# Kernel optimization log

Measured on AMD Instinct MI355X. Metric: run time of the kernel, lower is better.

Reference implementation:

```python
import jax, jax.numpy as jnp
import numpy as np

N_PARTICLES = 100000
STATE_DIM = 64          # 3 + 2*2 + 57
MSG_OUT = 64
HIDDEN = 32
N_EDGES = 1600000


def _init_linear(key, fan_in, fan_out):
    kw, kb = jax.random.split(key)
    bound = 1.0 / np.sqrt(fan_in)
    W = jax.random.uniform(kw, (fan_in, fan_out), minval=-bound, maxval=bound, dtype=jnp.float32)
    b = jax.random.uniform(kb, (fan_out,), minval=-bound, maxval=bound, dtype=jnp.float32)
    return W, b


def setup_inputs() -> dict:
    key = jax.random.key(0)
    ks = jax.random.split(key, 8)
    x = jax.random.normal(ks[0], (N_PARTICLES, STATE_DIM), dtype=jnp.float32)
    edge_index = jax.random.randint(ks[1], (2, N_EDGES), 0, N_PARTICLES, dtype=jnp.int64)
    # message conv MLP: [2*STATE_DIM] -> 32 -> 32 -> MSG_OUT
    mW1, mb1 = _init_linear(ks[2], 2 * STATE_DIM, HIDDEN)
    mW2, mb2 = _init_linear(ks[3], HIDDEN, HIDDEN)
    mW3, mb3 = _init_linear(ks[4], HIDDEN, MSG_OUT)
    # own_state_nn MLP: [STATE_DIM + MSG_OUT] -> 32 -> 32 -> STATE_DIM
    oW1, ob1 = _init_linear(ks[5], STATE_DIM + MSG_OUT, HIDDEN)
    oW2, ob2 = _init_linear(ks[6], HIDDEN, HIDDEN)
    oW3, ob3 = _init_linear(ks[7], HIDDEN, STATE_DIM)
    return {"x": x, "edge_index": edge_index,
            "mW1": mW1, "mb1": mb1, "mW2": mW2, "mb2": mb2, "mW3": mW3, "mb3": mb3,
            "oW1": oW1, "ob1": ob1, "oW2": oW2, "ob2": ob2, "oW3": oW3, "ob3": ob3}


def _mlp3(h, W1, b1, W2, b2, W3, b3):
    h = jax.nn.relu(h @ W1 + b1)
    h = jax.nn.relu(h @ W2 + b2)
    return h @ W3 + b3


def reference(x, edge_index, mW1, mb1, mW2, mb2, mW3, mb3,
              oW1, ob1, oW2, ob2, oW3, ob3):
    src, dst = edge_index[0], edge_index[1]
    # edge-wise message: MLP over [x_src || x_dst]  -> [E, MSG_OUT]
    e_feat = jnp.concatenate([x[src], x[dst]], axis=-1)  # [E, 2*STATE_DIM]
    m = _mlp3(e_feat, mW1, mb1, mW2, mb2, mW3, mb3)
    # scatter-sum aggregation at destination node
    messages = jax.ops.segment_sum(m, dst, num_segments=x.shape[0])  # [N, MSG_OUT]
    combined = jnp.concatenate([x, messages], axis=-1)  # [N, STATE_DIM+MSG_OUT]
    new_state = _mlp3(combined, oW1, ob1, oW2, ob2, oW3, ob3)
    return new_state
```

## Files before the change

kernel.cpp:

```cpp
#include <hip/hip_runtime.h>

#define NP 100000
#define NE 1600000
#define SD 64
#define HID 32
#define MSG 64
#define NP_PAD 100352
#define NTILE (NP / 16)
#define TILE_BLOCKS ((NTILE + 3) / 4)
#define BINSZ 512
#define NBIN ((NP + BINSZ - 1) / BINSZ)
#define EPW 8192
#define NWG ((NE + EPW - 1) / EPW)

typedef float v4f __attribute__((ext_vector_type(4)));
typedef short v4s __attribute__((ext_vector_type(4)));
typedef short v8s __attribute__((ext_vector_type(8)));
typedef __bf16 v8bf __attribute__((ext_vector_type(8)));

#define WQ_FRAGS 56

__device__ __forceinline__ v4f MFMA32(v8s a, v8s b, v4f c) {
  return __builtin_amdgcn_mfma_f32_16x16x32_bf16(
      __builtin_bit_cast(v8bf, a), __builtin_bit_cast(v8bf, b), c, 0, 0, 0);
}

__device__ __forceinline__ short f2bf(float f) {
  return __builtin_bit_cast(short, (__bf16)f);
}
__device__ __forceinline__ float bf2f(short s) {
  unsigned u = ((unsigned)(unsigned short)s) << 16;
  return __builtin_bit_cast(float, u);
}

__device__ __forceinline__ v4f mfma3(v8s ah, v8s al, v8s bh, v8s bl, v4f c) {
  c = MFMA32(al, bh, c);
  c = MFMA32(ah, bl, c);
  c = MFMA32(ah, bh, c);
  return c;
}

__device__ __forceinline__ void load_wfrag(const float* __restrict__ W, int ld,
                                           int kb, int m0, int lq, int l15,
                                           v8s* hi, v8s* lo) {
  v8s h, l;
#pragma unroll
  for (int j = 0; j < 8; ++j) {
    int k = kb + ((j < 4) ? (4 * lq + j) : (16 + 4 * lq + (j - 4)));
    float v = W[k * ld + m0 + l15];
    short hb = f2bf(v);
    h[j] = hb;
    l[j] = f2bf(v - bf2f(hb));
  }
  *hi = h;
  *lo = l;
}

__device__ __forceinline__ void split8(v4f a, v4f b, v8s* hi, v8s* lo) {
  v8s h, l;
#pragma unroll
  for (int j = 0; j < 4; ++j) {
    short ha = f2bf(a[j]); h[j] = ha; l[j] = f2bf(a[j] - bf2f(ha));
    short hb = f2bf(b[j]); h[j + 4] = hb; l[j + 4] = f2bf(b[j] - bf2f(hb));
  }
  *hi = h;
  *lo = l;
}

__device__ __forceinline__ void load_xfrag(const float* xs, int kb, int lq,
                                           v8s* hi, v8s* lo) {
  v4f a = *reinterpret_cast<const v4f*>(xs + kb + 4 * lq);
  v4f b = *reinterpret_cast<const v4f*>(xs + kb + 16 + 4 * lq);
  split8(a, b, hi, lo);
}

__device__ __forceinline__ void chain_frag(v4f d0, v4f d1, v8s* hi, v8s* lo) {
  v4f a, b;
#pragma unroll
  for (int j = 0; j < 4; ++j) {
    a[j] = fmaxf(d0[j], 0.f);
    b[j] = fmaxf(d1[j], 0.f);
  }
  split8(a, b, hi, lo);
}

__global__ __launch_bounds__(256, 2) void setup_kernel(
    const float* __restrict__ x, const int* __restrict__ ei,
    const float* __restrict__ mW1, const float* __restrict__ mb1,
    const float* __restrict__ mW2, const float* __restrict__ mW3,
    const float* __restrict__ oW1, const float* __restrict__ oW2,
    const float* __restrict__ oW3,
    int* __restrict__ gOff, short* __restrict__ wqs,
    float* __restrict__ h1d_buf, short* __restrict__ h1s_buf) {
  __shared__ int cnt[NBIN];
  const int blk = blockIdx.x;

  if (blk < NWG) {
    for (int i = threadIdx.x; i < NBIN; i += 256) cnt[i] = 0;
    __syncthreads();
    const int e0 = blk * EPW;
    const int e1 = (e0 + EPW < NE) ? e0 + EPW : NE;
    for (int e = e0 + threadIdx.x; e < e1; e += 256)
      atomicAdd(&cnt[ei[NE + e] >> 9], 1);
    __syncthreads();
    for (int i = threadIdx.x; i < NBIN; i += 256) gOff[i * NWG + blk] = cnt[i];
    return;
  }

  const int lane = threadIdx.x & 63;
  const int l15 = lane & 15;
  const int lq = lane >> 4;

  if (blk == NWG) {
    if (threadIdx.x >= 64) return;
    v8s* wq = reinterpret_cast<v8s*>(wqs);
    v8s h, l;
#pragma unroll
    for (int t = 0; t < 2; ++t)
#pragma unroll
      for (int kc = 0; kc < 2; ++kc) {
        load_wfrag(mW1, HID, kc * 32, t * 16, lq, l15, &h, &l);
        wq[(t * 2 + kc) * 64 + lane] = h;
        wq[(4 + t * 2 + kc) * 64 + lane] = l;
        load_wfrag(mW1, HID, 64 + kc * 32, t * 16, lq, l15, &h, &l);
        wq[(8 + t * 2 + kc) * 64 + lane] = h;
        wq[(12 + t * 2 + kc) * 64 + lane] = l;
      }
#pragma unroll
    for (int t = 0; t < 2; ++t) {
      load_wfrag(mW2, HID, 0, t * 16, lq, l15, &h, &l);
      wq[(16 + t) * 64 + lane] = h;
      wq[(18 + t) * 64 + lane] = l;
    }
#pragma unroll
    for (int t = 0; t < 4; ++t) {
      load_wfrag(mW3, MSG, 0, t * 16, lq, l15, &h, &l);
      wq[(20 + t) * 64 + lane] = h;
      wq[(24 + t) * 64 + lane] = l;
    }
#pragma unroll
    for (int t = 0; t < 2; ++t)
#pragma unroll
      for (int kc = 0; kc < 4; ++kc) {
        load_wfrag(oW1, HID, kc * 32, t * 16, lq, l15, &h, &l);
        wq[(28 + t * 4 + kc) * 64 + lane] = h;
        wq[(36 + t * 4 + kc) * 64 + lane] = l;
      }
#pragma unroll
    for (int t = 0; t < 2; ++t) {
      load_wfrag(oW2, HID, 0, t * 16, lq, l15, &h, &l);
      wq[(44 + t) * 64 + lane] = h;
      wq[(46 + t) * 64 + lane] = l;
    }
#pragma unroll
    for (int t = 0; t < 4; ++t) {
      load_wfrag(oW3, SD, 0, t * 16, lq, l15, &h, &l);
      wq[(48 + t) * 64 + lane] = h;
      wq[(52 + t) * 64 + lane] = l;
    }
    return;
  }

  const int tile = ((blk - NWG - 1) * 256 + (int)threadIdx.x) >> 6;
  if (tile >= NTILE) return;
  const int node = tile * 16 + l15;

  v4f d0, d1, s0 = {0.f, 0.f, 0.f, 0.f}, s1 = {0.f, 0.f, 0.f, 0.f};
#pragma unroll
  for (int q = 0; q < 4; ++q) {
    d0[q] = mb1[4 * lq + q];
    d1[q] = mb1[16 + 4 * lq + q];
  }
#pragma unroll
  for (int kc = 0; kc < 2; ++kc) {
    v8s xh, xl, wh, wl;
    load_xfrag(x + (size_t)node * SD, kc * 32, lq, &xh, &xl);
    load_wfrag(mW1, HID, 64 + kc * 32, 0, lq, l15, &wh, &wl);
    d0 = mfma3(wh, wl, xh, xl, d0);
    load_wfrag(mW1, HID, 64 + kc * 32, 16, lq, l15, &wh, &wl);
    d1 = mfma3(wh, wl, xh, xl, d1);
    load_wfrag(mW1, HID, kc * 32, 0, lq, l15, &wh, &wl);
    s0 = mfma3(wh, wl, xh, xl, s0);
    load_wfrag(mW1, HID, kc * 32, 16, lq, l15, &wh, &wl);
    s1 = mfma3(wh, wl, xh, xl, s1);
  }
  *reinterpret_cast<v4f*>(h1d_buf + (size_t)node * HID + 4 * lq) = d0;
  *reinterpret_cast<v4f*>(h1d_buf + (size_t)node * HID + 16 + 4 * lq) = d1;
  v4s q0, q1;
#pragma unroll
  for (int q = 0; q < 4; ++q) {
    q0[q] = f2bf(s0[q]);
    q1[q] = f2bf(s1[q]);
  }
  *reinterpret_cast<v4s*>(h1s_buf + (size_t)node * HID + 4 * lq) = q0;
  *reinterpret_cast<v4s*>(h1s_buf + (size_t)node * HID + 16 + 4 * lq) = q1;
}


__global__ __launch_bounds__(256) void scan_bins_kernel(
    int* __restrict__ gOff, int* __restrict__ binStart) {
  __shared__ int tot[NBIN];
  const int b = threadIdx.x;
  if (b < NBIN) {
    int run = 0;
    for (int w = 0; w < NWG; ++w) {
      int v = gOff[b * NWG + w];
      gOff[b * NWG + w] = run;
      run += v;
    }
    tot[b] = run;
  }
  __syncthreads();
  if (threadIdx.x == 0) {
    int run = 0;
    for (int bb = 0; bb < NBIN; ++bb) {
      binStart[bb] = run;
      run += tot[bb];
    }
    binStart[NBIN] = run;
  }
  __syncthreads();
  if (b < NBIN) {
    int base = binStart[b];
    for (int w = 0; w < NWG; ++w) gOff[b * NWG + w] += base;
  }
}

__global__ __launch_bounds__(256) void bin_scatter_kernel(
    const int* __restrict__ ei, const int* __restrict__ gOff,
    int2* __restrict__ pairs) {
  __shared__ int cur[NBIN];
  const int w = blockIdx.x;
  for (int i = threadIdx.x; i < NBIN; i += 256) cur[i] = gOff[i * NWG + w];
  __syncthreads();
  const int e0 = w * EPW;
  const int e1 = (e0 + EPW < NE) ? e0 + EPW : NE;
  for (int e = e0 + threadIdx.x; e < e1; e += 256) {
    int s = ei[e];
    int d = ei[NE + e];
    int pos = atomicAdd(&cur[d >> 9], 1);
    pairs[pos] = make_int2(s, d);
  }
}

__global__ __launch_bounds__(512) void bin_csr_kernel(
    const int2* __restrict__ pairs, const int* __restrict__ binStart,
    int2* __restrict__ co, int* __restrict__ csr_src) {
  __shared__ int sh[BINSZ];
  __shared__ int cu[BINSZ];
  const int b = blockIdx.x;
  const int t = threadIdx.x;
  cu[t] = 0;
  __syncthreads();
  const int p0 = binStart[b], p1 = binStart[b + 1];
  for (int p = p0 + t; p < p1; p += BINSZ)
    atomicAdd(&cu[pairs[p].y & (BINSZ - 1)], 1);
  __syncthreads();
  const int v = cu[t];
  sh[t] = v;
  __syncthreads();
  for (int off = 1; off < BINSZ; off <<= 1) {
    int a = (t >= off) ? sh[t - off] : 0;
    __syncthreads();
    sh[t] += a;
    __syncthreads();
  }
  const int excl = sh[t] - v;
  const int node = b * BINSZ + t;
  if (node < NP) co[node] = make_int2(p0 + excl, v);
  cu[t] = excl;
  __syncthreads();
  for (int p = p0 + t; p < p1; p += BINSZ) {
    int2 pr = pairs[p];
    int loc = atomicAdd(&cu[pr.y & (BINSZ - 1)], 1);
    csr_src[p0 + loc] = pr.x;
  }
}

__global__ __launch_bounds__(256, 4) void edge_mfma_kernel(
    const short* __restrict__ h1s, const float* __restrict__ h1d_buf,
    const short* __restrict__ wqs, const int2* __restrict__ co,
    const int* __restrict__ csr_src, const float* __restrict__ mb2,
    float* __restrict__ rsum) {
  const int lane = threadIdx.x & 63;
  const int l15 = lane & 15;
  const int lq = lane >> 4;
  const int wid = (blockIdx.x * 256 + threadIdx.x) >> 6;
  const int nw = gridDim.x * 4;
  const v8s* wq = reinterpret_cast<const v8s*>(wqs);

  const v8s w2h0 = wq[16 * 64 + lane], w2h1 = wq[17 * 64 + lane];
  const v8s w2l0 = wq[18 * 64 + lane], w2l1 = wq[19 * 64 + lane];
  v4f bb0, bb1;
#pragma unroll
  for (int q = 0; q < 4; ++q) {
    bb0[q] = mb2[4 * lq + q];
    bb1[q] = mb2[16 + 4 * lq + q];
  }

  for (int n = wid; n < NP; n += nw) {
    const int2 c = co[n];
    const int off = c.x, cnt = c.y;
    const int ng = (cnt + 15) >> 4;

    const v4f h1d0 = *reinterpret_cast<const v4f*>(h1d_buf + (size_t)n * HID + 4 * lq);
    const v4f h1d1 = *reinterpret_cast<const v4f*>(h1d_buf + (size_t)n * HID + 16 + 4 * lq);

    v4f r0 = {0.f, 0.f, 0.f, 0.f}, r1 = {0.f, 0.f, 0.f, 0.f};

    int sa = (l15 < cnt) ? csr_src[off + l15] : 0;
    v4s a0 = *reinterpret_cast<const v4s*>(h1s + (size_t)sa * HID + 4 * lq);
    v4s b0 = *reinterpret_cast<const v4s*>(h1s + (size_t)sa * HID + 16 + 4 * lq);
    int sb = (l15 < cnt - 16) ? csr_src[off + 16 + l15] : 0;
    v4s a1 = *reinterpret_cast<const v4s*>(h1s + (size_t)sb * HID + 4 * lq);
    v4s b1 = *reinterpret_cast<const v4s*>(h1s + (size_t)sb * HID + 16 + 4 * lq);

    int rem = cnt;
    for (int g = 0; g < ng; ++g) {
      int sc = (l15 < rem - 32) ? csr_src[off + (g + 2) * 16 + l15] : 0;

      v4f d0, d1;
#pragma unroll
      for (int q = 0; q < 4; ++q) {
        d0[q] = h1d0[q] + bf2f(a0[q]);
        d1[q] = h1d1[q] + bf2f(b0[q]);
      }

      v8s ph, pl;
      chain_frag(d0, d1, &ph, &pl);
      v4f e0 = bb0, e1 = bb1;
      e0 = mfma3(w2h0, w2l0, ph, pl, e0);
      e1 = mfma3(w2h1, w2l1, ph, pl, e1);

      if (l15 < rem) {
#pragma unroll
        for (int j = 0; j < 4; ++j) {
          r0[j] += fmaxf(e0[j], 0.f);
          r1[j] += fmaxf(e1[j], 0.f);
        }
      }

      v4s a2 = *reinterpret_cast<const v4s*>(h1s + (size_t)sc * HID + 4 * lq);
      v4s b2 = *reinterpret_cast<const v4s*>(h1s + (size_t)sc * HID + 16 + 4 * lq);

      a0 = a1; b0 = b1;
      a1 = a2; b1 = b2;
      rem -= 16;
    }

#pragma unroll
    for (int j = 0; j < 4; ++j) {
      float a = r0[j], b = r1[j];
      a += __shfl_xor(a, 1); a += __shfl_xor(a, 2);
      a += __shfl_xor(a, 4); a += __shfl_xor(a, 8);
      b += __shfl_xor(b, 1); b += __shfl_xor(b, 2);
      b += __shfl_xor(b, 4); b += __shfl_xor(b, 8);
      r0[j] = a; r1[j] = b;
    }
    if (l15 == 0) {
      *reinterpret_cast<v4f*>(rsum + (size_t)n * HID + 4 * lq) = r0;
      *reinterpret_cast<v4f*>(rsum + (size_t)n * HID + 16 + 4 * lq) = r1;
    }
  }
}

__global__ __launch_bounds__(256, 2) void fused_tail_kernel(
    const float* __restrict__ x, const short* __restrict__ wqs,
    const float* __restrict__ rsum, const int2* __restrict__ co,
    const float* __restrict__ mb3,
    const float* __restrict__ ob1, const float* __restrict__ ob2,
    const float* __restrict__ ob3,
    float* __restrict__ out) {
  const int lane = threadIdx.x & 63;
  const int l15 = lane & 15;
  const int lq = lane >> 4;
  const int tile = (blockIdx.x * 256 + threadIdx.x) >> 6;
  if (tile >= NTILE) return;
  const v8s* wq = reinterpret_cast<const v8s*>(wqs);

  const int node = tile * 16 + l15;
  const float fc = (float)co[node].y;

  v4f ra = *reinterpret_cast<const v4f*>(rsum + (size_t)node * HID + 4 * lq);
  v4f rb = *reinterpret_cast<const v4f*>(rsum + (size_t)node * HID + 16 + 4 * lq);
  v8s bh, bl;
  split8(ra, rb, &bh, &bl);

  v4f m[4];
#pragma unroll
  for (int t = 0; t < 4; ++t) {
    v4f c = {0.f, 0.f, 0.f, 0.f};
    c = mfma3(wq[(20 + t) * 64 + lane], wq[(24 + t) * 64 + lane], bh, bl, c);
#pragma unroll
    for (int q = 0; q < 4; ++q) c[q] += fc * mb3[t * 16 + 4 * lq + q];
    m[t] = c;
  }

  v4f d0, d1;
#pragma unroll
  for (int q = 0; q < 4; ++q) {
    d0[q] = ob1[4 * lq + q];
    d1[q] = ob1[16 + 4 * lq + q];
  }
#pragma unroll
  for (int kc = 0; kc < 2; ++kc) {
    v8s xh, xl;
    load_xfrag(x + (size_t)node * SD, kc * 32, lq, &xh, &xl);
    d0 = mfma3(wq[(28 + kc) * 64 + lane], wq[(36 + kc) * 64 + lane], xh, xl, d0);
    d1 = mfma3(wq[(32 + kc) * 64 + lane], wq[(40 + kc) * 64 + lane], xh, xl, d1);
  }
#pragma unroll
  for (int kc = 0; kc < 2; ++kc) {
    v8s mh, ml;
    split8(m[kc * 2], m[kc * 2 + 1], &mh, &ml);
    d0 = mfma3(wq[(30 + kc) * 64 + lane], wq[(38 + kc) * 64 + lane], mh, ml, d0);
    d1 = mfma3(wq[(34 + kc) * 64 + lane], wq[(42 + kc) * 64 + lane], mh, ml, d1);
  }

  v8s ph, pl;
  chain_frag(d0, d1, &ph, &pl);
  v4f e0, e1;
#pragma unroll
  for (int q = 0; q < 4; ++q) {
    e0[q] = ob2[4 * lq + q];
    e1[q] = ob2[16 + 4 * lq + q];
  }
  e0 = mfma3(wq[44 * 64 + lane], wq[46 * 64 + lane], ph, pl, e0);
  e1 = mfma3(wq[45 * 64 + lane], wq[47 * 64 + lane], ph, pl, e1);

  v8s rh, rl;
  chain_frag(e0, e1, &rh, &rl);
  float* orow = out + (size_t)node * SD;
#pragma unroll
  for (int t = 0; t < 4; ++t) {
    v4f c;
#pragma unroll
    for (int q = 0; q < 4; ++q) c[q] = ob3[t * 16 + 4 * lq + q];
    c = mfma3(wq[(48 + t) * 64 + lane], wq[(52 + t) * 64 + lane], rh, rl, c);
    *reinterpret_cast<v4f*>(orow + t * 16 + 4 * lq) = c;
  }
}

extern "C" void kernel_launch(void* const* d_in, const int* in_sizes, int n_in,
                              void* d_out, int out_size, void* d_ws,
                              size_t ws_size, hipStream_t stream) {
  const float* x = (const float*)d_in[0];
  const int* ei = (const int*)d_in[1];
  const float* mW1 = (const float*)d_in[2];
  const float* mb1 = (const float*)d_in[3];
  const float* mW2 = (const float*)d_in[4];
  const float* mb2 = (const float*)d_in[5];
  const float* mW3 = (const float*)d_in[6];
  const float* mb3 = (const float*)d_in[7];
  const float* oW1 = (const float*)d_in[8];
  const float* ob1 = (const float*)d_in[9];
  const float* oW2 = (const float*)d_in[10];
  const float* ob2 = (const float*)d_in[11];
  const float* oW3 = (const float*)d_in[12];
  const float* ob3 = (const float*)d_in[13];
  float* out = (float*)d_out;

  float* h1d_buf = (float*)d_out;
  short* h1s_buf = (short*)((char*)d_out + (size_t)NP * HID * 4);

  char* p = (char*)d_ws;
  short* wqs = (short*)p;            p += (size_t)WQ_FRAGS * 64 * 16;
  int* gOff = (int*)p;               p += (size_t)NBIN * NWG * 4;
  int* binStart = (int*)p;           p += 200 * 4;
  int2* co = (int2*)p;               p += (size_t)NP_PAD * 8;
  int* csr_src = (int*)p;            p += (size_t)NE * 4;
  int2* pairs = (int2*)p;
  float* rsum = (float*)pairs;

  setup_kernel<<<NWG + 1 + TILE_BLOCKS, 256, 0, stream>>>(
      x, ei, mW1, mb1, mW2, mW3, oW1, oW2, oW3, gOff, wqs, h1d_buf, h1s_buf);

  scan_bins_kernel<<<1, 256, 0, stream>>>(gOff, binStart);
  bin_scatter_kernel<<<NWG, 256, 0, stream>>>(ei, gOff, pairs);
  bin_csr_kernel<<<NBIN, 512, 0, stream>>>(pairs, binStart, co, csr_src);

  edge_mfma_kernel<<<2048, 256, 0, stream>>>(
      h1s_buf, h1d_buf, wqs, co, csr_src, mb2, rsum);

  fused_tail_kernel<<<TILE_BLOCKS, 256, 0, stream>>>(
      x, wqs, rsum, co, mb3, ob1, ob2, ob3, out);
}
```

Before: 158.1 us.

## Prefetch next node's CSR offsets in edge kernel; vectorize and parallelize bin scan

The edge MFMA kernel now loads the next node's CSR offset/count, its first neighbour index and that neighbour's features during the current node's work. This hides the dependent-load latency at the start of each node. Launch bounds rise to 6 waves per SIMD and the grid drops from 2048 to 1536 blocks, which may pressure registers. The bin scan kernel now reads rows as int4 and uses a parallel Hillis-Steele scan across bins instead of a single-thread loop. That scan relies on NWG being divisible by 4 and on int4 alignment.

```diff
diff --git a/kernel.cpp b/kernel.cpp
--- a/kernel.cpp
+++ b/kernel.cpp
@@ -199,30 +199,40 @@
 
 __global__ __launch_bounds__(256) void scan_bins_kernel(
     int* __restrict__ gOff, int* __restrict__ binStart) {
-  __shared__ int tot[NBIN];
+  __shared__ int sh[256];
   const int b = threadIdx.x;
+  int run = 0;
   if (b < NBIN) {
-    int run = 0;
-    for (int w = 0; w < NWG; ++w) {
-      int v = gOff[b * NWG + w];
-      gOff[b * NWG + w] = run;
-      run += v;
-    }
-    tot[b] = run;
-  }
+    int4* row = reinterpret_cast<int4*>(gOff + b * NWG);
+#pragma unroll 4
+    for (int i = 0; i < NWG / 4; ++i) {
+      int4 v = row[i];
+      int4 w;
+      w.x = run; run += v.x;
+      w.y = run; run += v.y;
+      w.z = run; run += v.z;
+      w.w = run; run += v.w;
+      row[i] = w;
+    }
+  }
+  sh[b] = run;
   __syncthreads();
-  if (threadIdx.x == 0) {
-    int run = 0;
-    for (int bb = 0; bb < NBIN; ++bb) {
-      binStart[bb] = run;
-      run += tot[bb];
-    }
-    binStart[NBIN] = run;
-  }
-  __syncthreads();
+  for (int off = 1; off < 256; off <<= 1) {
+    int a = (b >= off) ? sh[b - off] : 0;
+    __syncthreads();
+    sh[b] += a;
+    __syncthreads();
+  }
+  const int excl = sh[b] - run;
+  if (b <= NBIN) binStart[b] = excl;
   if (b < NBIN) {
-    int base = binStart[b];
-    for (int w = 0; w < NWG; ++w) gOff[b * NWG + w] += base;
+    int4* row = reinterpret_cast<int4*>(gOff + b * NWG);
+#pragma unroll 4
+    for (int i = 0; i < NWG / 4; ++i) {
+      int4 v = row[i];
+      v.x += excl; v.y += excl; v.z += excl; v.w += excl;
+      row[i] = v;
+    }
   }
 }
 
@@ -277,7 +287,7 @@
   }
 }
 
-__global__ __launch_bounds__(256, 4) void edge_mfma_kernel(
+__global__ __launch_bounds__(256, 6) void edge_mfma_kernel(
     const short* __restrict__ h1s, const float* __restrict__ h1d_buf,
     const short* __restrict__ wqs, const int2* __restrict__ co,
     const int* __restrict__ csr_src, const float* __restrict__ mb2,
@@ -298,22 +308,32 @@
     bb1[q] = mb2[16 + 4 * lq + q];
   }
 
+  int2 c_cur = make_int2(0, 0);
+  v4s a0c = {0, 0, 0, 0}, b0c = {0, 0, 0, 0};
+  if (wid < NP) {
+    c_cur = co[wid];
+    int sa = (l15 < c_cur.y) ? csr_src[c_cur.x + l15] : 0;
+    a0c = *reinterpret_cast<const v4s*>(h1s + (size_t)sa * HID + 4 * lq);
+    b0c = *reinterpret_cast<const v4s*>(h1s + (size_t)sa * HID + 16 + 4 * lq);
+  }
+
   for (int n = wid; n < NP; n += nw) {
-    const int2 c = co[n];
-    const int off = c.x, cnt = c.y;
+    const int off = c_cur.x, cnt = c_cur.y;
     const int ng = (cnt + 15) >> 4;
+    const int nn = n + nw;
+
+    int2 cnx = make_int2(0, 0);
+    if (nn < NP) cnx = co[nn];
 
     const v4f h1d0 = *reinterpret_cast<const v4f*>(h1d_buf + (size_t)n * HID + 4 * lq);
     const v4f h1d1 = *reinterpret_cast<const v4f*>(h1d_buf + (size_t)n * HID + 16 + 4 * lq);
 
-    v4f r0 = {0.f, 0.f, 0.f, 0.f}, r1 = {0.f, 0.f, 0.f, 0.f};
-
-    int sa = (l15 < cnt) ? csr_src[off + l15] : 0;
-    v4s a0 = *reinterpret_cast<const v4s*>(h1s + (size_t)sa * HID + 4 * lq);
-    v4s b0 = *reinterpret_cast<const v4s*>(h1s + (size_t)sa * HID + 16 + 4 * lq);
+    v4s a0 = a0c, b0 = b0c;
     int sb = (l15 < cnt - 16) ? csr_src[off + 16 + l15] : 0;
     v4s a1 = *reinterpret_cast<const v4s*>(h1s + (size_t)sb * HID + 4 * lq);
     v4s b1 = *reinterpret_cast<const v4s*>(h1s + (size_t)sb * HID + 16 + 4 * lq);
+
+    v4f r0 = {0.f, 0.f, 0.f, 0.f}, r1 = {0.f, 0.f, 0.f, 0.f};
 
     int rem = cnt;
     for (int g = 0; g < ng; ++g) {
@@ -347,6 +367,9 @@
       a1 = a2; b1 = b2;
       rem -= 16;
     }
+
+    int san = 0;
+    if (nn < NP) san = (l15 < cnx.y) ? csr_src[cnx.x + l15] : 0;
 
 #pragma unroll
     for (int j = 0; j < 4; ++j) {
@@ -361,6 +384,10 @@
       *reinterpret_cast<v4f*>(rsum + (size_t)n * HID + 4 * lq) = r0;
       *reinterpret_cast<v4f*>(rsum + (size_t)n * HID + 16 + 4 * lq) = r1;
     }
+
+    c_cur = cnx;
+    a0c = *reinterpret_cast<const v4s*>(h1s + (size_t)san * HID + 4 * lq);
+    b0c = *reinterpret_cast<const v4s*>(h1s + (size_t)san * HID + 16 + 4 * lq);
   }
 }
 
@@ -479,7 +506,7 @@
   bin_scatter_kernel<<<NWG, 256, 0, stream>>>(ei, gOff, pairs);
   bin_csr_kernel<<<NBIN, 512, 0, stream>>>(pairs, binStart, co, csr_src);
 
-  edge_mfma_kernel<<<2048, 256, 0, stream>>>(
+  edge_mfma_kernel<<<1536, 256, 0, stream>>>(
       h1s_buf, h1d_buf, wqs, co, csr_src, mb2, rsum);
 
   fused_tail_kernel<<<TILE_BLOCKS, 256, 0, stream>>>(
```

Measured after the change: 182.4 us. 15.4% more time.
